# Kernel optimization log

Hardware: AMD Instinct MI355X
Metric: run time of the kernel (lower is better)

The kernel has to match this reference:

```python
import jax, jax.numpy as jnp
import numpy as np
from jax import lax

B, L, D = 4, 4096, 1024
K = 4          # kernel_size
E = 2          # expand_dim
C = D * E      # expanded channels


def setup_inputs() -> dict:
    key = jax.random.key(0)
    ks = jax.random.split(key, 6)
    s_in = 1.0 / np.sqrt(D)
    s_ex = 1.0 / np.sqrt(C)
    s_cv = 1.0 / np.sqrt(K)  # torch Conv1d init: 1/sqrt(in_ch/groups * k) = 1/sqrt(k) for depthwise
    return {
        "x": jax.random.normal(ks[0], (B, L, D), dtype=jnp.float32),
        "W_exp": jax.random.uniform(ks[1], (D, C), jnp.float32, -s_in, s_in),
        "b_exp": jax.random.uniform(ks[2], (C,), jnp.float32, -s_in, s_in),
        "conv_w": jax.random.uniform(ks[3], (K, 1, C), jnp.float32, -s_cv, s_cv),  # LIO layout
        "conv_b": jax.random.uniform(ks[4], (C,), jnp.float32, -s_cv, s_cv),
        "W_cmp": jax.random.uniform(ks[5], (C, D), jnp.float32, -s_ex, s_ex),
        "b_cmp": jax.random.uniform(jax.random.fold_in(key, 7), (D,), jnp.float32, -s_ex, s_ex),
    }


def reference(x, W_exp, b_exp, conv_w, conv_b, W_cmp, b_cmp):
    # expand: (b,l,d) -> (b,l,C)
    xe = x @ W_exp + b_exp
    # depthwise causal conv over length: left-pad K-1 (equivalent to torch
    # padding=K-1 on both sides followed by [..., :l] slice)
    y = lax.conv_general_dilated(
        xe, conv_w,
        window_strides=(1,),
        padding=[(K - 1, 0)],
        dimension_numbers=("NLC", "LIO", "NLC"),
        feature_group_count=C,
    ) + conv_b
    # compress: (b,l,C) -> (b,l,d)
    return y @ W_cmp + b_cmp
```

## Files before the change

kernel.cpp:

```cpp
#include <hip/hip_runtime.h>
#include <stdint.h>

#define B_ 4
#define L_ 4096
#define D_ 1024
#define C_ 2048
#define M_ (B_ * L_)
#define LCH 16

typedef __attribute__((ext_vector_type(8))) short s16x8;
typedef __attribute__((ext_vector_type(4))) float fx4;
typedef unsigned short bfu;

__device__ __forceinline__ float bits2f(short s) {
  return __uint_as_float(((uint32_t)(unsigned short)s) << 16);
}
__device__ __forceinline__ bfu f2bf(float f) {
  uint32_t u = __float_as_uint(f);
  uint32_t r = (u + 0x7FFFu + ((u >> 16) & 1u)) >> 16;
  return (bfu)r;
}

__device__ __forceinline__ void gload_lds16(const void* g, void* l) {
  __builtin_amdgcn_global_load_lds(
      (const __attribute__((address_space(1))) void*)g,
      (__attribute__((address_space(3))) void*)l, 16, 0, 0);
}

#define BAR() asm volatile("s_barrier" ::: "memory")
#define LGKM0() asm volatile("s_waitcnt lgkmcnt(0)" ::: "memory")
#define VMW4() asm volatile("s_waitcnt vmcnt(4)" ::: "memory")
#define VMW0() asm volatile("s_waitcnt vmcnt(0)" ::: "memory")

__global__ __launch_bounds__(256) void cvt_f32_bf16(const float* __restrict__ in,
                                                    bfu* __restrict__ out, int n8) {
  const int stride = gridDim.x * blockDim.x;
  for (int i = blockIdx.x * blockDim.x + threadIdx.x; i < n8; i += stride) {
    const size_t off = (size_t)i * 8;
    fx4 a = *(const fx4*)(in + off);
    fx4 b = *(const fx4*)(in + off + 4);
    s16x8 o;
#pragma unroll
    for (int j = 0; j < 4; j++) {
      o[j] = (short)f2bf(a[j]);
      o[j + 4] = (short)f2bf(b[j]);
    }
    *reinterpret_cast<s16x8*>(out + off) = o;
  }
}

template <int R, int CC>
__global__ __launch_bounds__(256) void transpose_cvt(const float* __restrict__ in,
                                                     bfu* __restrict__ out) {
  __shared__ float tile[32][33];
  const int bx = blockIdx.x, by = blockIdx.y, tx = threadIdx.x;
  for (int j = threadIdx.y; j < 32; j += 8)
    tile[j][tx] = in[(size_t)(by * 32 + j) * CC + bx * 32 + tx];
  __syncthreads();
  for (int j = threadIdx.y; j < 32; j += 8)
    out[(size_t)(bx * 32 + j) * R + by * 32 + tx] = f2bf(tile[tx][j]);
}


__device__ __forceinline__ s16x8 lfrag(const bfu* region, int row, int lg) {
  const int lin = row * 64 + lg * 16;
  const int swz = lin ^ ((lin >> 3) & 48);
  return *reinterpret_cast<const s16x8*>(reinterpret_cast<const char*>(region) + swz);
}

template <int KD>
__device__ __forceinline__ void stage_half(const bfu* __restrict__ Mt, int r0, int kb,
                                           bfu* region, int t) {
#pragma unroll
  for (int h = 0; h < 2; h++) {
    const int u = t + h * 512;
    const int srow = u >> 2;
    const int sslot = (u & 3) ^ ((srow >> 1) & 3);
    gload_lds16(Mt + (size_t)(r0 + srow) * KD + kb + sslot * 8, region + u * 8);
  }
}

template <int N, int KD, bool OUT_BF16>
__global__ __launch_bounds__(512, 2) void gemm256(const bfu* __restrict__ A,
                                                  const bfu* __restrict__ Bt,
                                                  const float* __restrict__ bias,
                                                  void* __restrict__ Cptr) {
  __shared__ bfu lds[2 * 4 * 8192];
  const int t = threadIdx.x;
  const int lane = t & 63, wid = t >> 6;
  const int wr = wid >> 2, wc = wid & 3;
  const int lr = lane & 15, lg = lane >> 4;
  const int cpx = gridDim.x >> 3;
  const int li = (blockIdx.x & 7) * cpx + (blockIdx.x >> 3);
  const int row0 = (li % (M_ / 256)) * 256;
  const int col0 = (li / (M_ / 256)) * 256;
  constexpr int ntk = KD / 64;

  fx4 acc[8][4] = {};

  stage_half<KD>(A, row0, 0, lds + 0, t);
  stage_half<KD>(Bt, col0, 0, lds + 16384, t);
  stage_half<KD>(A, row0, 32, lds + 8192, t);
  stage_half<KD>(Bt, col0, 32, lds + 24576, t);
  stage_half<KD>(A, row0, 64, lds + 32768 + 0, t);
  stage_half<KD>(Bt, col0, 64, lds + 32768 + 16384, t);
  VMW4();
  BAR();

  for (int tau = 0; tau < ntk; ++tau) {
    bfu* cb_ = (tau & 1) ? lds + 32768 : lds;
    bfu* nb_ = (tau & 1) ? lds : lds + 32768;
    const int ar = wr * 128 + lr;
    const int br = wc * 64 + lr;
    s16x8 af[4], bf4[4];

#pragma unroll
    for (int m = 0; m < 4; m++) af[m] = lfrag(cb_ + 0, ar + m * 16, lg);
#pragma unroll
    for (int n = 0; n < 4; n++) bf4[n] = lfrag(cb_ + 16384, br + n * 16, lg);
    if (tau + 1 < ntk) stage_half<KD>(A, row0, (tau + 1) * 64 + 32, nb_ + 8192, t);
    BAR();
    LGKM0();
    __builtin_amdgcn_s_setprio(1);
#pragma unroll
    for (int m = 0; m < 4; m++)
#pragma unroll
      for (int n = 0; n < 4; n++)
        acc[m][n] = __builtin_amdgcn_mfma_f32_16x16x32_bf16(af[m], bf4[n], acc[m][n], 0, 0, 0);
    __builtin_amdgcn_s_setprio(0);
    BAR();

#pragma unroll
    for (int m = 0; m < 4; m++) af[m] = lfrag(cb_ + 0, ar + 64 + m * 16, lg);
    if (tau + 1 < ntk) stage_half<KD>(Bt, col0, (tau + 1) * 64 + 32, nb_ + 24576, t);
    BAR();
    LGKM0();
    __builtin_amdgcn_s_setprio(1);
#pragma unroll
    for (int m = 0; m < 4; m++)
#pragma unroll
      for (int n = 0; n < 4; n++)
        acc[m + 4][n] = __builtin_amdgcn_mfma_f32_16x16x32_bf16(af[m], bf4[n], acc[m + 4][n], 0, 0, 0);
    __builtin_amdgcn_s_setprio(0);
    BAR();

#pragma unroll
    for (int m = 0; m < 4; m++) af[m] = lfrag(cb_ + 8192, ar + m * 16, lg);
#pragma unroll
    for (int n = 0; n < 4; n++) bf4[n] = lfrag(cb_ + 24576, br + n * 16, lg);
    if (tau + 2 < ntk) stage_half<KD>(A, row0, (tau + 2) * 64, cb_ + 0, t);
    BAR();
    LGKM0();
    __builtin_amdgcn_s_setprio(1);
#pragma unroll
    for (int m = 0; m < 4; m++)
#pragma unroll
      for (int n = 0; n < 4; n++)
        acc[m][n] = __builtin_amdgcn_mfma_f32_16x16x32_bf16(af[m], bf4[n], acc[m][n], 0, 0, 0);
    __builtin_amdgcn_s_setprio(0);
    BAR();

#pragma unroll
    for (int m = 0; m < 4; m++) af[m] = lfrag(cb_ + 8192, ar + 64 + m * 16, lg);
    if (tau + 2 < ntk) stage_half<KD>(Bt, col0, (tau + 2) * 64, cb_ + 16384, t);
    BAR();
    LGKM0();
    __builtin_amdgcn_s_setprio(1);
#pragma unroll
    for (int m = 0; m < 4; m++)
#pragma unroll
      for (int n = 0; n < 4; n++)
        acc[m + 4][n] = __builtin_amdgcn_mfma_f32_16x16x32_bf16(af[m], bf4[n], acc[m + 4][n], 0, 0, 0);
    __builtin_amdgcn_s_setprio(0);
    if (tau < ntk - 1) {
      if (tau < ntk - 2) VMW4();
      else VMW0();
    }
    BAR();
  }

  float bv[4];
#pragma unroll
  for (int n = 0; n < 4; n++) bv[n] = bias[col0 + wc * 64 + n * 16 + lr];
#pragma unroll
  for (int m = 0; m < 8; m++)
#pragma unroll
    for (int n = 0; n < 4; n++)
#pragma unroll
      for (int r = 0; r < 4; r++) {
        const int row = row0 + wr * 128 + m * 16 + lg * 4 + r;
        const int col = col0 + wc * 64 + n * 16 + lr;
        const float v = acc[m][n][r] + bv[n];
        if constexpr (OUT_BF16)
          ((bfu*)Cptr)[(size_t)row * N + col] = f2bf(v);
        else
          ((float*)Cptr)[(size_t)row * N + col] = v;
      }
}

__global__ __launch_bounds__(256) void dwconv_slide(const bfu* __restrict__ xe,
                                                    const float* __restrict__ cw,
                                                    const float* __restrict__ cb,
                                                    bfu* __restrict__ y) {
  const int nchunk = L_ / LCH;
  const int b = blockIdx.x / nchunk;
  const int l0 = (blockIdx.x % nchunk) * LCH;
  const int cg = threadIdx.x << 3;

  float w[4][8], bias8[8];
#pragma unroll
  for (int tt = 0; tt < 4; tt++) {
    fx4 w0 = *(const fx4*)(cw + tt * C_ + cg);
    fx4 w1 = *(const fx4*)(cw + tt * C_ + cg + 4);
#pragma unroll
    for (int i = 0; i < 4; i++) {
      w[tt][i] = w0[i];
      w[tt][i + 4] = w1[i];
    }
  }
  {
    fx4 c0 = *(const fx4*)(cb + cg), c1 = *(const fx4*)(cb + cg + 4);
#pragma unroll
    for (int i = 0; i < 4; i++) {
      bias8[i] = c0[i];
      bias8[i + 4] = c1[i];
    }
  }

  const size_t base = ((size_t)b * L_ + l0) * C_ + cg;
  s16x8 h0 = {}, h1 = {}, h2 = {};
  if (l0 != 0) {
    h0 = *reinterpret_cast<const s16x8*>(xe + base - 3 * C_);
    h1 = *reinterpret_cast<const s16x8*>(xe + base - 2 * C_);
    h2 = *reinterpret_cast<const s16x8*>(xe + base - 1 * C_);
  }
#pragma unroll
  for (int i = 0; i < LCH; i++) {
    s16x8 h3 = *reinterpret_cast<const s16x8*>(xe + base + (size_t)i * C_);
    s16x8 o;
#pragma unroll
    for (int j = 0; j < 8; j++) {
      float v = bias8[j];
      v = fmaf(bits2f(h0[j]), w[0][j], v);
      v = fmaf(bits2f(h1[j]), w[1][j], v);
      v = fmaf(bits2f(h2[j]), w[2][j], v);
      v = fmaf(bits2f(h3[j]), w[3][j], v);
      o[j] = (short)f2bf(v);
    }
    *reinterpret_cast<s16x8*>(y + base + (size_t)i * C_) = o;
    h0 = h1;
    h1 = h2;
    h2 = h3;
  }
}

extern "C" void kernel_launch(void* const* d_in, const int* in_sizes, int n_in,
                              void* d_out, int out_size, void* d_ws, size_t ws_size,
                              hipStream_t stream) {
  const float* x = (const float*)d_in[0];
  const float* W_exp = (const float*)d_in[1];
  const float* b_exp = (const float*)d_in[2];
  const float* cw = (const float*)d_in[3];
  const float* cb = (const float*)d_in[4];
  const float* W_cmp = (const float*)d_in[5];
  const float* b_cmp = (const float*)d_in[6];
  float* out = (float*)d_out;

  char* ws = (char*)d_ws;
  bfu* wexp_t = (bfu*)(ws);
  bfu* wcmp_t = (bfu*)(ws + (4u << 20));
  bfu* xb = (bfu*)(ws + (8u << 20));
  bfu* xe = (bfu*)(ws + (40u << 20));
  bfu* y = (bfu*)(ws + (104u << 20));

  cvt_f32_bf16<<<2048, 256, 0, stream>>>(x, xb, M_ * D_ / 8);
  transpose_cvt<D_, C_><<<dim3(C_ / 32, D_ / 32), dim3(32, 8), 0, stream>>>(W_exp, wexp_t);
  transpose_cvt<C_, D_><<<dim3(D_ / 32, C_ / 32), dim3(32, 8), 0, stream>>>(W_cmp, wcmp_t);
  gemm256<C_, D_, true><<<512, 512, 0, stream>>>(xb, wexp_t, b_exp, xe);
  dwconv_slide<<<B_ * (L_ / LCH), 256, 0, stream>>>(xe, cw, cb, y);
  gemm256<D_, C_, false><<<256, 512, 0, stream>>>(y, wcmp_t, b_cmp, out);
}
```

Before: 201.0 us.

## Add 256x128 double-buffered GEMM kernel for compress stage and precompute LDS offsets

Adds a new gemm_bulk kernel with 256 threads and a 256x128 output tile that double-buffers 32-wide K slices. It is used for the compress GEMM so that 512 blocks are launched instead of 256, which should give the 256 CUs better occupancy and load balance. The existing gemm256 now uses precomputed swizzled LDS byte offsets instead of calling lfrag for each fragment, which cuts address arithmetic. The trade-off is that the new kernel waits on all outstanding loads every iteration and reuses less data per block.

Result: slower. 219.2 us (+9.0%).

```diff
diff --git a/kernel.cpp b/kernel.cpp
--- a/kernel.cpp
+++ b/kernel.cpp
@@ -80,7 +80,22 @@
   }
 }
 
-template <int N, int KD, bool OUT_BF16>
+template <int KD, int NR>
+__device__ __forceinline__ void stage_rows256(const bfu* __restrict__ Mt, int r0, int kb,
+                                              bfu* region, int t) {
+#pragma unroll
+  for (int h = 0; h < NR / 64; h++) {
+    const int u = t + h * 256;
+    const int srow = u >> 2;
+    const int sslot = (u & 3) ^ ((srow >> 1) & 3);
+    gload_lds16(Mt + (size_t)(r0 + srow) * KD + kb + sslot * 8, region + u * 8);
+  }
+}
+
+#define LF(bytoff) \
+  (*reinterpret_cast<const s16x8*>(reinterpret_cast<const char*>(lds) + (bytoff)))
+
+template <int MM, int N, int KD, bool OUT_BF16>
 __global__ __launch_bounds__(512, 2) void gemm256(const bfu* __restrict__ A,
                                                   const bfu* __restrict__ Bt,
                                                   const float* __restrict__ bias,
@@ -92,9 +107,11 @@
   const int lr = lane & 15, lg = lane >> 4;
   const int cpx = gridDim.x >> 3;
   const int li = (blockIdx.x & 7) * cpx + (blockIdx.x >> 3);
-  const int row0 = (li % (M_ / 256)) * 256;
-  const int col0 = (li / (M_ / 256)) * 256;
+  const int row0 = (li % (MM / 256)) * 256;
+  const int col0 = (li / (MM / 256)) * 256;
   constexpr int ntk = KD / 64;
+  const int abase = ((wr * 128 + lr) * 64 + lg * 16) ^ (((lr >> 1) & 3) << 4);
+  const int bbase = ((wc * 64 + lr) * 64 + lg * 16) ^ (((lr >> 1) & 3) << 4);
 
   fx4 acc[8][4] = {};
 
@@ -108,16 +125,14 @@
   BAR();
 
   for (int tau = 0; tau < ntk; ++tau) {
-    bfu* cb_ = (tau & 1) ? lds + 32768 : lds;
+    const int cbb = (tau & 1) ? 65536 : 0;
     bfu* nb_ = (tau & 1) ? lds : lds + 32768;
-    const int ar = wr * 128 + lr;
-    const int br = wc * 64 + lr;
     s16x8 af[4], bf4[4];
 
 #pragma unroll
-    for (int m = 0; m < 4; m++) af[m] = lfrag(cb_ + 0, ar + m * 16, lg);
-#pragma unroll
-    for (int n = 0; n < 4; n++) bf4[n] = lfrag(cb_ + 16384, br + n * 16, lg);
+    for (int m = 0; m < 4; m++) af[m] = LF(cbb + abase + m * 1024);
+#pragma unroll
+    for (int n = 0; n < 4; n++) bf4[n] = LF(cbb + 32768 + bbase + n * 1024);
     if (tau + 1 < ntk) stage_half<KD>(A, row0, (tau + 1) * 64 + 32, nb_ + 8192, t);
     BAR();
     LGKM0();
@@ -131,7 +146,7 @@
     BAR();
 
 #pragma unroll
-    for (int m = 0; m < 4; m++) af[m] = lfrag(cb_ + 0, ar + 64 + m * 16, lg);
+    for (int m = 0; m < 4; m++) af[m] = LF(cbb + abase + 4096 + m * 1024);
     if (tau + 1 < ntk) stage_half<KD>(Bt, col0, (tau + 1) * 64 + 32, nb_ + 24576, t);
     BAR();
     LGKM0();
@@ -145,10 +160,10 @@
     BAR();
 
 #pragma unroll
-    for (int m = 0; m < 4; m++) af[m] = lfrag(cb_ + 8192, ar + m * 16, lg);
-#pragma unroll
-    for (int n = 0; n < 4; n++) bf4[n] = lfrag(cb_ + 24576, br + n * 16, lg);
-    if (tau + 2 < ntk) stage_half<KD>(A, row0, (tau + 2) * 64, cb_ + 0, t);
+    for (int m = 0; m < 4; m++) af[m] = LF(cbb + 16384 + abase + m * 1024);
+#pragma unroll
+    for (int n = 0; n < 4; n++) bf4[n] = LF(cbb + 49152 + bbase + n * 1024);
+    if (tau + 2 < ntk) stage_half<KD>(A, row0, (tau + 2) * 64, lds + (cbb >> 1), t);
     BAR();
     LGKM0();
     __builtin_amdgcn_s_setprio(1);
@@ -161,8 +176,8 @@
     BAR();
 
 #pragma unroll
-    for (int m = 0; m < 4; m++) af[m] = lfrag(cb_ + 8192, ar + 64 + m * 16, lg);
-    if (tau + 2 < ntk) stage_half<KD>(Bt, col0, (tau + 2) * 64, cb_ + 16384, t);
+    for (int m = 0; m < 4; m++) af[m] = LF(cbb + 16384 + abase + 4096 + m * 1024);
+    if (tau + 2 < ntk) stage_half<KD>(Bt, col0, (tau + 2) * 64, lds + (cbb >> 1) + 16384, t);
     BAR();
     LGKM0();
     __builtin_amdgcn_s_setprio(1);
@@ -176,6 +191,74 @@
       if (tau < ntk - 2) VMW4();
       else VMW0();
     }
+    BAR();
+  }
+
+  float bv[4];
+#pragma unroll
+  for (int n = 0; n < 4; n++) bv[n] = bias[col0 + wc * 64 + n * 16 + lr];
+#pragma unroll
+  for (int m = 0; m < 8; m++)
+#pragma unroll
+    for (int n = 0; n < 4; n++)
+#pragma unroll
+      for (int r = 0; r < 4; r++) {
+        const int row = row0 + wr * 128 + m * 16 + lg * 4 + r;
+        const int col = col0 + wc * 64 + n * 16 + lr;
+        const float v = acc[m][n][r] + bv[n];
+        if constexpr (OUT_BF16)
+          ((bfu*)Cptr)[(size_t)row * N + col] = f2bf(v);
+        else
+          ((float*)Cptr)[(size_t)row * N + col] = v;
+      }
+}
+
+template <int MM, int N, int KD, bool OUT_BF16>
+__global__ __launch_bounds__(256, 2) void gemm_bulk(const bfu* __restrict__ A,
+                                                    const bfu* __restrict__ Bt,
+                                                    const float* __restrict__ bias,
+                                                    void* __restrict__ Cptr) {
+  __shared__ bfu lds[24576];
+  const int t = threadIdx.x;
+  const int lane = t & 63, wid = t >> 6;
+  const int wr = wid >> 1, wc = wid & 1;
+  const int lr = lane & 15, lg = lane >> 4;
+  const int cpx = gridDim.x >> 3;
+  const int li = (blockIdx.x & 7) * cpx + (blockIdx.x >> 3);
+  const int row0 = (li % (MM / 256)) * 256;
+  const int col0 = (li / (MM / 256)) * 128;
+  constexpr int ntk = KD / 32;
+  const int abase = ((wr * 128 + lr) * 64 + lg * 16) ^ (((lr >> 1) & 3) << 4);
+  const int bbase = 16384 + (((wc * 64 + lr) * 64 + lg * 16) ^ (((lr >> 1) & 3) << 4));
+
+  fx4 acc[8][4] = {};
+
+  stage_rows256<KD, 256>(A, row0, 0, lds + 0, t);
+  stage_rows256<KD, 128>(Bt, col0, 0, lds + 8192, t);
+  VMW0();
+  BAR();
+
+  for (int tau = 0; tau < ntk; ++tau) {
+    const int cbb = (tau & 1) ? 24576 : 0;
+    bfu* nb_ = (tau & 1) ? lds : lds + 12288;
+    if (tau + 1 < ntk) {
+      stage_rows256<KD, 256>(A, row0, (tau + 1) * 32, nb_ + 0, t);
+      stage_rows256<KD, 128>(Bt, col0, (tau + 1) * 32, nb_ + 8192, t);
+    }
+    s16x8 af[8], bf4[4];
+#pragma unroll
+    for (int m = 0; m < 8; m++) af[m] = LF(cbb + abase + m * 1024);
+#pragma unroll
+    for (int n = 0; n < 4; n++) bf4[n] = LF(cbb + bbase + n * 1024);
+    __builtin_amdgcn_s_setprio(1);
+#pragma unroll
+    for (int m = 0; m < 8; m++)
+#pragma unroll
+      for (int n = 0; n < 4; n++)
+        acc[m][n] = __builtin_amdgcn_mfma_f32_16x16x32_bf16(af[m], bf4[n], acc[m][n], 0, 0, 0);
+    __builtin_amdgcn_s_setprio(0);
+    LGKM0();
+    VMW0();
     BAR();
   }
 
@@ -276,7 +359,7 @@
   cvt_f32_bf16<<<2048, 256, 0, stream>>>(x, xb, M_ * D_ / 8);
   transpose_cvt<D_, C_><<<dim3(C_ / 32, D_ / 32), dim3(32, 8), 0, stream>>>(W_exp, wexp_t);
   transpose_cvt<C_, D_><<<dim3(D_ / 32, C_ / 32), dim3(32, 8), 0, stream>>>(W_cmp, wcmp_t);
-  gemm256<C_, D_, true><<<512, 512, 0, stream>>>(xb, wexp_t, b_exp, xe);
+  gemm256<M_, C_, D_, true><<<512, 512, 0, stream>>>(xb, wexp_t, b_exp, xe);
   dwconv_slide<<<B_ * (L_ / LCH), 256, 0, stream>>>(xe, cw, cb, y);
-  gemm256<D_, C_, false><<<256, 512, 0, stream>>>(y, wcmp_t, b_cmp, out);
-}
+  gemm_bulk<M_, D_, C_, false><<<512, 256, 0, stream>>>(y, wcmp_t, b_cmp, out);
+}
```
